# Kernel tuning notes

Hardware: AMD Instinct MI355X
Metric: run time of the kernel (lower is better)

Reference implementation:

```python
import jax, jax.numpy as jnp
from jax import lax
import numpy as np

B, H, W = 16, 512, 512
OPENING_R, EROSION_R, DILATION_R = 5, 2, 1
MIN_SIZE, AREA_THRESHOLD = 2000, 300
INF = np.int32(2 ** 30)


def _disk(r):
    # skimage.morphology.disk: x^2 + y^2 <= r^2 on a (2r+1)^2 grid
    y, x = np.mgrid[-r:r + 1, -r:r + 1]
    return jnp.asarray((x * x + y * y <= r * r).astype(np.float32))


D_OPEN, D_ERODE, D_DILATE = _disk(OPENING_R), _disk(EROSION_R), _disk(DILATION_R)


def _conv2(x, k):
    return lax.conv_general_dilated(x[None, None], k[None, None], (1, 1), 'VALID')[0, 0]


def _erode(fg, se):
    # skimage binary_erosion uses border_value=True (image border does not erode)
    r = se.shape[0] // 2
    x = jnp.pad(fg.astype(jnp.float32), r, constant_values=1.0)
    return _conv2(x, se) >= se.sum() - 0.5


def _dilate(fg, se):
    # skimage binary_dilation uses border_value=False
    r = se.shape[0] // 2
    x = jnp.pad(fg.astype(jnp.float32), r, constant_values=0.0)
    return _conv2(x, se) > 0.5


def _seg_cummin(v, reset, axis, reverse):
    # segmented cumulative-min: scan resets wherever `reset` is True (background)
    def comb(a, b):
        av, af = a
        bv, bf = b
        return jnp.where(bf, bv, jnp.minimum(av, bv)), af | bf

    vv, _ = lax.associative_scan(comb, (v, reset), axis=axis, reverse=reverse)
    return vv


def _label(fg):
    # 4-connectivity connected-component labeling via min-label propagation.
    # Each fg pixel starts with its raveled index; alternating row/col segmented
    # cummin sweeps run under while_loop until a fixed point (root id per comp).
    h, w = fg.shape
    idx = jnp.arange(h * w, dtype=jnp.int32).reshape(h, w)
    lab0 = jnp.where(fg, idx, INF)
    bg = ~fg

    def sweep(l):
        for axis in (1, 0):
            for rev in (False, True):
                l = jnp.where(fg, _seg_cummin(l, bg, axis, rev), INF)
        return l

    def body(c):
        l, _ = c
        nl = sweep(l)
        return nl, jnp.array_equal(nl, l)

    lab, _ = lax.while_loop(lambda c: ~c[1], body, (lab0, jnp.array(False)))
    seg = jnp.where(fg, lab, 0).ravel()
    sizes = jax.ops.segment_sum(fg.astype(jnp.int32).ravel(), seg, num_segments=h * w)
    ncomp = jnp.sum(sizes > 0)
    return lab, sizes, ncomp


def _remove_small_objects(fg, min_size, guard):
    lab, sizes, ncomp = _label(fg)
    px = sizes[jnp.where(fg, lab, 0)]  # component size at every fg pixel
    kept = fg & (px >= min_size)
    # original only removes small objects when label(...).max() > 1
    return jnp.where(ncomp > 1, kept, fg) if guard else kept


def _pipeline(mask):
    fg = mask > 0
    fg = _remove_small_objects(fg, MIN_SIZE, True)
    # remove_small_holes == ~remove_small_objects(~fg, area_threshold + 1)
    fg = ~_remove_small_objects(~fg, AREA_THRESHOLD + 1, False)
    fg = _erode(fg, D_ERODE)
    fg = _dilate(_erode(fg, D_OPEN), D_OPEN)  # binary_opening
    fg = _remove_small_objects(fg, MIN_SIZE, True)
    fg = _dilate(fg, D_DILATE)
    return fg.astype(jnp.float32)  # original casts to int; float32 kept for vjp parity


def setup_inputs() -> dict:
    key = jax.random.key(0)
    # blobby binary masks: threshold bilinearly-upsampled low-res noise so that
    # realistic large connected components (> min_size px) exist
    low = jax.random.uniform(key, (B, H // 16, W // 16), dtype=jnp.float32)
    blob = jax.image.resize(low, (B, H, W), method='bilinear')
    return {'inputs': (blob > 0.5).astype(jnp.float32)}


def reference(inputs):
    return jax.vmap(_pipeline)(inputs)
```

## Files before the change

### kernel.cpp

```cpp
#include <hip/hip_runtime.h>
#include <stdint.h>

#define BATCH 16
#define H 512
#define W 512
#define HW (H * W)
#define NTOT (BATCH * HW)
#define NWORDS (NTOT / 64)

#define TPB 256
#define NBLKW ((NWORDS + TPB - 1) / TPB)

#define SROWS 16
#define SWORDS 128
#define SPIX 8192
#define NSTRIPS (NWORDS / SWORDS)

__device__ __forceinline__ int find_root_c(int* L, int x) {
    int r = x, p = L[r];
    while (p != r) { r = p; p = L[r]; }
    if (L[x] != r) atomicMin(&L[x], r);
    return r;
}

__device__ void merge_uf(int* L, int a, int b) {
    while (true) {
        a = find_root_c(L, a);
        b = find_root_c(L, b);
        if (a == b) return;
        int lo = a < b ? a : b;
        int hi = a < b ? b : a;
        int old = atomicMin(&L[hi], lo);
        if (old == hi) return;
        a = lo; b = old;
    }
}

__device__ __forceinline__ int find_root_lds(int* P, int x) {
    int r = x, p = P[r];
    while (p != r) { r = p; p = P[r]; }
    return r;
}

__device__ void merge_lds(int* P, int a, int b) {
    while (true) {
        a = find_root_lds(P, a);
        b = find_root_lds(P, b);
        if (a == b) return;
        int lo = a < b ? a : b;
        int hi = a < b ? b : a;
        int old = atomicMin(&P[hi], lo);
        if (old == hi) return;
        a = lo; b = old;
    }
}

__device__ __forceinline__ int start_of(uint64_t m, int i, int cv, int base) {
    uint64_t below = i ? ((~m) & ((1ull << i) - 1)) : 0ull;
    if (below == 0) return (cv >= 0) ? cv : base;
    int hz = 63 - __builtin_clzll(below);
    return base + hz + 1;
}

__device__ uint64_t keep_word(const uint64_t* __restrict__ bits,
                              const int* __restrict__ carry, const int* __restrict__ L,
                              const int* __restrict__ sizes, const int* __restrict__ ncomp,
                              int minsz, int gw) {
    uint64_t m = bits[gw];
    uint64_t res = m;
    if (m && ncomp[gw >> 12] > 1) {
        int cv = carry[gw];
        int base = gw << 6;
        while (m) {
            int s = __builtin_ctzll(m);
            uint64_t rest = m >> s;
            uint64_t nr = ~rest;
            int len = nr ? __builtin_ctzll(nr) : (64 - s);
            uint64_t piece = ((len >= 64) ? ~0ull : ((1ull << len) - 1)) << s;
            int start = (s == 0 && cv >= 0) ? cv : (base + s);
            if (sizes[L[start]] < minsz) res &= ~piece;
            m &= ~piece;
        }
    }
    return res;
}

__device__ uint64_t fill_word(const uint64_t* __restrict__ bits,
                              const int* __restrict__ carry, const int* __restrict__ L,
                              const int* __restrict__ sizes, int minsz, int gw) {
    uint64_t fg = bits[gw];
    uint64_t bg = ~fg;
    uint64_t res = fg;
    int cv = carry[gw];
    int base = gw << 6;
    while (bg) {
        int s = __builtin_ctzll(bg);
        uint64_t rest = bg >> s;
        uint64_t nr = ~rest;
        int len = nr ? __builtin_ctzll(nr) : (64 - s);
        uint64_t piece = ((len >= 64) ? ~0ull : ((1ull << len) - 1)) << s;
        int start = (s == 0 && cv >= 0) ? cv : (base + s);
        if (sizes[L[start]] < minsz) res |= piece;
        bg &= ~piece;
    }
    return res;
}

template <int R, bool ERODE>
__device__ uint64_t morph_word_lds(const uint64_t* buf, int lrow, int w, int gyTop) {
    const uint64_t BORDER = ERODE ? ~0ull : 0ull;
    uint64_t res = ERODE ? ~0ull : 0ull;
#pragma unroll
    for (int dy = -R; dy <= R; ++dy) {
        int lr = lrow + dy;
        int gy = gyTop + lr;
        if (gy < 0 || gy >= H) continue;
        int v = R * R - dy * dy;
        int kx = 0;
        while ((kx + 1) * (kx + 1) <= v) ++kx;
        uint64_t cur = buf[lr * 8 + w];
        uint64_t prv = (w > 0) ? buf[lr * 8 + w - 1] : BORDER;
        uint64_t nxt = (w < 7) ? buf[lr * 8 + w + 1] : BORDER;
        uint64_t acc = cur;
#pragma unroll
        for (int dx = 1; dx <= kx; ++dx) {
            uint64_t right = (cur >> dx) | (nxt << (64 - dx));
            uint64_t left  = (cur << dx) | (prv >> (64 - dx));
            if (ERODE) acc &= right & left;
            else       acc |= right | left;
        }
        if (ERODE) res &= acc;
        else       res |= acc;
    }
    return res;
}

__device__ void strip_ccl_body(uint64_t m, uint64_t* sw, int* scarry, int* par,
                               int blk, int t,
                               int* __restrict__ carry, int* __restrict__ L,
                               int* __restrict__ sizes, int* __restrict__ ncomp) {
    sw[t] = m;
    __syncthreads();

    if (t < SROWS) {
        int cv = -1;
        for (int i = 0; i < 8; ++i) {
            int lw = t * 8 + i;
            scarry[lw] = cv;
            uint64_t w = sw[lw];
            if (w >> 63) {
                uint64_t z = ~w;
                if (z == 0) { if (cv < 0) cv = lw << 6; }
                else { int hz = 63 - __builtin_clzll(z); cv = (lw << 6) + hz + 1; }
            } else cv = -1;
        }
    }
    __syncthreads();

    int cv = scarry[t];
    carry[blk * SWORDS + t] = (cv >= 0) ? (blk * SPIX + cv) : -1;
    int lbase = t << 6;
    uint64_t starts = m & ~((m << 1) | ((cv >= 0) ? 1ull : 0ull));
    uint64_t ss = starts;
    while (ss) {
        int s = __builtin_ctzll(ss);
        par[lbase + s] = lbase + s;
        ss &= ss - 1;
    }
    __syncthreads();

    if (t >= 8 && m) {
        uint64_t up = sw[t - 8];
        uint64_t cand = m & up;
        if (cand) {
            uint64_t curprev = (t & 7) ? sw[t - 1] : 0ull;
            uint64_t upprev  = (t & 7) ? sw[t - 9] : 0ull;
            uint64_t curl = (m << 1) | (curprev >> 63);
            uint64_t upl  = (up << 1) | (upprev >> 63);
            cand &= ~(curl & upl);
            int cvu = scarry[t - 8];
            while (cand) {
                int i = __builtin_ctzll(cand);
                int sP = start_of(m, i, cv, lbase);
                int sQ = start_of(up, i, cvu, lbase - 512);
                merge_lds(par, sP, sQ);
                cand &= cand - 1;
            }
        }
    }
    __syncthreads();

    int gpix = blk * SPIX;
    ss = starts;
    while (ss) {
        int s = __builtin_ctzll(ss);
        int ls = lbase + s;
        int r = find_root_lds(par, ls);
        L[gpix + ls] = gpix + r;
        if (r == ls) sizes[gpix + ls] = 0;
        ss &= ss - 1;
    }
    if (t == 0 && (blk & 31) == 0) ncomp[blk >> 5] = 0;
}


__global__ void k_thresh_pack4(const float4* __restrict__ in4,
                               uint64_t* __restrict__ bits) {
    int q = blockIdx.x * blockDim.x + threadIdx.x;
    if (q >= NTOT / 4) return;
    float4 v = in4[q];
    uint32_t nib = (v.x > 0.0f ? 1u : 0u) | (v.y > 0.0f ? 2u : 0u) |
                   (v.z > 0.0f ? 4u : 0u) | (v.w > 0.0f ? 8u : 0u);
    uint64_t val = (uint64_t)nib << (4 * (threadIdx.x & 15));
    val |= __shfl_xor(val, 1);
    val |= __shfl_xor(val, 2);
    val |= __shfl_xor(val, 4);
    val |= __shfl_xor(val, 8);
    if ((threadIdx.x & 15) == 0) bits[q >> 4] = val;
}

__global__ void k_strip_ccl(const uint64_t* __restrict__ bits, int inv,
                            int* __restrict__ carry, int* __restrict__ L,
                            int* __restrict__ sizes, int* __restrict__ ncomp) {
    __shared__ uint64_t sw[SWORDS];
    __shared__ int scarry[SWORDS];
    __shared__ int par[SPIX];
    int blk = blockIdx.x;
    int t = threadIdx.x;
    uint64_t inv64 = inv ? ~0ull : 0ull;
    uint64_t m = bits[blk * SWORDS + t] ^ inv64;
    strip_ccl_body(m, sw, scarry, par, blk, t, carry, L, sizes, ncomp);
}

__global__ void k_keep_strip(const uint64_t* __restrict__ bits,
                             const int* __restrict__ carryIn, const int* __restrict__ Lin,
                             const int* __restrict__ sizesIn, const int* __restrict__ ncompIn,
                             uint64_t* __restrict__ outBits,
                             int* __restrict__ carryOut, int* __restrict__ Lout,
                             int* __restrict__ sizesOut, int* __restrict__ ncompOut) {
    __shared__ uint64_t sw[SWORDS];
    __shared__ int scarry[SWORDS];
    __shared__ int par[SPIX];
    int blk = blockIdx.x;
    int t = threadIdx.x;
    int gw = blk * SWORDS + t;
    uint64_t kw = keep_word(bits, carryIn, Lin, sizesIn, ncompIn, 2000, gw);
    outBits[gw] = kw;
    strip_ccl_body(~kw, sw, scarry, par, blk, t, carryOut, Lout, sizesOut, ncompOut);
}

__global__ void k_merge_bound(const uint64_t* __restrict__ bits, int inv,
                              const int* __restrict__ carry, int* __restrict__ L) {
    int tid = threadIdx.x;
    if (tid >= 248) return;
    int img = blockIdx.x;
    int y = ((tid >> 3) + 1) * SROWS;
    int w = tid & 7;
    int gw = img * 4096 + y * 8 + w;
    uint64_t inv64 = inv ? ~0ull : 0ull;
    uint64_t cur = bits[gw] ^ inv64;
    uint64_t up  = bits[gw - 8] ^ inv64;
    uint64_t cand = cur & up;
    if (!cand) return;
    uint64_t curprev = w ? (bits[gw - 1] ^ inv64) : 0ull;
    uint64_t upprev  = w ? (bits[gw - 9] ^ inv64) : 0ull;
    uint64_t curl = (cur << 1) | (curprev >> 63);
    uint64_t upl  = (up << 1)  | (upprev >> 63);
    cand &= ~(curl & upl);
    if (!cand) return;
    int cvc = carry[gw], cvu = carry[gw - 8];
    int base = gw << 6;
    while (cand) {
        int i = __builtin_ctzll(cand);
        int sP = start_of(cur, i, cvc, base);
        int sQ = start_of(up, i, cvu, base - W);
        merge_uf(L, sP, sQ);
        cand &= cand - 1;
    }
}

__global__ void k_flatten_count(const uint64_t* __restrict__ bits, int inv,
                                const int* __restrict__ carry, int* __restrict__ L,
                                int* __restrict__ sizes, int* __restrict__ ncomp) {
    __shared__ int hk[128];
    __shared__ int hv[128];
    for (int i = threadIdx.x; i < 128; i += TPB) { hk[i] = -1; hv[i] = 0; }
    __syncthreads();

    int gw = blockIdx.x * blockDim.x + threadIdx.x;
    if (gw < NWORDS) {
        uint64_t inv64 = inv ? ~0ull : 0ull;
        uint64_t m = bits[gw] ^ inv64;
        if (m) {
            int cv = carry[gw];
            int base = gw << 6;
            while (m) {
                int s = __builtin_ctzll(m);
                uint64_t rest = m >> s;
                uint64_t nr = ~rest;
                int len = nr ? __builtin_ctzll(nr) : (64 - s);
                uint64_t piece = ((len >= 64) ? ~0ull : ((1ull << len) - 1)) << s;
                bool initial = !(s == 0 && cv >= 0);
                int start = initial ? (base + s) : cv;
                int r = find_root_c(L, start);
                if (initial && r == start) atomicAdd(&ncomp[gw >> 12], 1);
                int cnt = __popcll(piece);
                uint32_t h = ((uint32_t)r * 2654435761u) >> 25;
                bool done = false;
                for (int tt = 0; tt < 16; ++tt) {
                    int slot = (h + tt) & 127;
                    int k = hk[slot];
                    if (k == -1) k = atomicCAS(&hk[slot], -1, r);
                    if (k == -1 || k == r) { atomicAdd(&hv[slot], cnt); done = true; break; }
                }
                if (!done) atomicAdd(&sizes[r], cnt);
                m &= ~piece;
            }
        }
    }
    __syncthreads();
    for (int i = threadIdx.x; i < 128; i += TPB)
        if (hk[i] != -1) atomicAdd(&sizes[hk[i]], hv[i]);
}

__global__ void k_fill_morph_ccl(const uint64_t* __restrict__ bits,
                                 const int* __restrict__ carryB, const int* __restrict__ LB,
                                 const int* __restrict__ sizesB,
                                 uint64_t* __restrict__ bits3,
                                 int* __restrict__ carryA, int* __restrict__ LA,
                                 int* __restrict__ sizesA, int* __restrict__ ncompA) {
    __shared__ uint64_t sw[SWORDS];
    __shared__ int scarry[SWORDS];
    __shared__ union {
        int par[SPIX];
        struct { uint64_t A[320]; uint64_t B[320]; } mo;
    } U;
    int s = blockIdx.x;
    int t = threadIdx.x;
    int img = s >> 5, si = s & 31;
    int gyTop = si * 16 - 12;

    for (int lw = t; lw < 320; lw += SWORDS) {
        int gy = gyTop + (lw >> 3);
        int w = lw & 7;
        uint64_t v = 0;
        if (gy >= 0 && gy < H)
            v = fill_word(bits, carryB, LB, sizesB, 301, img * 4096 + gy * 8 + w);
        U.mo.A[lw] = v;
    }
    __syncthreads();
    for (int lw = t; lw < 320; lw += SWORDS) {
        int lr = lw >> 3;
        if (lr >= 2 && lr <= 37) U.mo.B[lw] = morph_word_lds<2, true>(U.mo.A, lr, lw & 7, gyTop);
    }
    __syncthreads();
    for (int lw = t; lw < 320; lw += SWORDS) {
        int lr = lw >> 3;
        if (lr >= 7 && lr <= 32) U.mo.A[lw] = morph_word_lds<5, true>(U.mo.B, lr, lw & 7, gyTop);
    }
    __syncthreads();
    for (int lw = t; lw < 320; lw += SWORDS) {
        int lr = lw >> 3;
        if (lr >= 12 && lr <= 27) U.mo.B[lw] = morph_word_lds<5, false>(U.mo.A, lr, lw & 7, gyTop);
    }
    __syncthreads();
    uint64_t m3 = U.mo.B[t + 96];
    bits3[s * SWORDS + t] = m3;
    strip_ccl_body(m3, sw, scarry, U.par, s, t, carryA, LA, sizesA, ncompA);
}

__global__ void k_keep_dilate_float(const uint64_t* __restrict__ bits,
                                    const int* __restrict__ carry, const int* __restrict__ L,
                                    const int* __restrict__ sizes, const int* __restrict__ ncomp,
                                    float* __restrict__ out) {
    __shared__ uint64_t kb[10 * 8];
    __shared__ uint64_t db[8 * 8];
    int blk = blockIdx.x;
    int img = blk >> 6;
    int s = blk & 63;
    int y0 = s * 8;
    int t = threadIdx.x;

    if (t < 80) {
        int lr = t >> 3;
        int w = t & 7;
        int gy = y0 - 1 + lr;
        uint64_t v = 0;
        if (gy >= 0 && gy < H)
            v = keep_word(bits, carry, L, sizes, ncomp, 2000, img * 4096 + gy * 8 + w);
        kb[t] = v;
    }
    __syncthreads();
    if (t < 64) {
        int r = t >> 3, w = t & 7;
        uint64_t cur = kb[(r + 1) * 8 + w];
        uint64_t up  = kb[r * 8 + w];
        uint64_t dn  = kb[(r + 2) * 8 + w];
        uint64_t prv = w ? kb[(r + 1) * 8 + w - 1] : 0ull;
        uint64_t nxt = (w < 7) ? kb[(r + 1) * 8 + w + 1] : 0ull;
        db[t] = cur | up | dn | (cur << 1) | (prv >> 63) | (cur >> 1) | (nxt << 63);
    }
    __syncthreads();

    int q0 = t * 16;
    uint64_t wd = db[q0 >> 6];
    int sh = q0 & 63;
    float4* o = (float4*)(out + (size_t)img * HW + (size_t)y0 * W + q0);
#pragma unroll
    for (int k = 0; k < 4; ++k) {
        uint32_t nib = (uint32_t)(wd >> (sh + k * 4)) & 0xFu;
        float4 f;
        f.x = (nib & 1u) ? 1.0f : 0.0f;
        f.y = (nib & 2u) ? 1.0f : 0.0f;
        f.z = (nib & 4u) ? 1.0f : 0.0f;
        f.w = (nib & 8u) ? 1.0f : 0.0f;
        o[k] = f;
    }
}

extern "C" void kernel_launch(void* const* d_in, const int* in_sizes, int n_in,
                              void* d_out, int out_size, void* d_ws, size_t ws_size,
                              hipStream_t stream) {
    const float* in = (const float*)d_in[0];
    float* out = (float*)d_out;

    uint8_t* ws = (uint8_t*)d_ws;
    int* LA      = (int*)ws;
    int* sizesA  = (int*)(ws + (size_t)NTOT * 4);
    int* LB      = (int*)(ws + (size_t)NTOT * 8);
    int* sizesB  = (int*)(ws + (size_t)NTOT * 12);
    uint64_t* bits1 = (uint64_t*)(ws + (size_t)NTOT * 16);
    uint64_t* bits2 = bits1 + NWORDS;
    uint64_t* bits3 = bits2 + NWORDS;
    int* carryA = (int*)(bits3 + NWORDS);
    int* carryB = carryA + NWORDS;
    int* ncompA = carryB + NWORDS;
    int* ncompB = ncompA + BATCH;

    k_thresh_pack4<<<(NTOT / 4 + TPB - 1) / TPB, TPB, 0, stream>>>((const float4*)in, bits1);

    k_strip_ccl<<<NSTRIPS, SWORDS, 0, stream>>>(bits1, 0, carryA, LA, sizesA, ncompA);
    k_merge_bound<<<BATCH, 256, 0, stream>>>(bits1, 0, carryA, LA);
    k_flatten_count<<<NBLKW, TPB, 0, stream>>>(bits1, 0, carryA, LA, sizesA, ncompA);

    k_keep_strip<<<NSTRIPS, SWORDS, 0, stream>>>(bits1, carryA, LA, sizesA, ncompA,
                                                 bits2, carryB, LB, sizesB, ncompB);
    k_merge_bound<<<BATCH, 256, 0, stream>>>(bits2, 1, carryB, LB);
    k_flatten_count<<<NBLKW, TPB, 0, stream>>>(bits2, 1, carryB, LB, sizesB, ncompB);

    k_fill_morph_ccl<<<NSTRIPS, SWORDS, 0, stream>>>(bits2, carryB, LB, sizesB,
                                                     bits3, carryA, LA, sizesA, ncompA);
    k_merge_bound<<<BATCH, 256, 0, stream>>>(bits3, 0, carryA, LA);
    k_flatten_count<<<NBLKW, TPB, 0, stream>>>(bits3, 0, carryA, LA, sizesA, ncompA);

    k_keep_dilate_float<<<BATCH * 64, TPB, 0, stream>>>(bits3, carryA, LA, sizesA, ncompA, out);
}
```

Baseline: 201.3 us.

## Fuse all pipeline stages into one cooperative kernel with grid syncs

Replaces eleven separate kernel launches with a single cooperative persistent kernel of 512 blocks. Stages are separated by grid.sync(), and shared memory is reused through a union. The aim is to remove per-launch overhead and inter-kernel gaps, since the workload is small. In exchange, each stage runs under a fixed 512-block geometry, boundary merges are spread as 8 items per block, and every grid barrier has its own cost. The old multi-kernel path stays as a fallback if the cooperative launch fails.

```diff
diff --git a/kernel.cpp b/kernel.cpp
--- a/kernel.cpp
+++ b/kernel.cpp
@@ -1,5 +1,8 @@
 #include <hip/hip_runtime.h>
+#include <hip/hip_cooperative_groups.h>
 #include <stdint.h>
+
+namespace cg = cooperative_groups;
 
 #define BATCH 16
 #define H 512
@@ -15,6 +18,7 @@
 #define SWORDS 128
 #define SPIX 8192
 #define NSTRIPS (NWORDS / SWORDS)
+#define NBOUND (BATCH * 248)
 
 __device__ __forceinline__ int find_root_c(int* L, int x) {
     int r = x, p = L[r];
@@ -139,7 +143,7 @@
                                int blk, int t,
                                int* __restrict__ carry, int* __restrict__ L,
                                int* __restrict__ sizes, int* __restrict__ ncomp) {
-    sw[t] = m;
+    if (t < SWORDS) sw[t] = m;
     __syncthreads();
 
     if (t < SROWS) {
@@ -157,19 +161,23 @@
     }
     __syncthreads();
 
-    int cv = scarry[t];
-    carry[blk * SWORDS + t] = (cv >= 0) ? (blk * SPIX + cv) : -1;
     int lbase = t << 6;
-    uint64_t starts = m & ~((m << 1) | ((cv >= 0) ? 1ull : 0ull));
-    uint64_t ss = starts;
-    while (ss) {
-        int s = __builtin_ctzll(ss);
-        par[lbase + s] = lbase + s;
-        ss &= ss - 1;
-    }
-    __syncthreads();
-
-    if (t >= 8 && m) {
+    int cv = -1;
+    uint64_t starts = 0ull;
+    if (t < SWORDS) {
+        cv = scarry[t];
+        carry[blk * SWORDS + t] = (cv >= 0) ? (blk * SPIX + cv) : -1;
+        starts = m & ~((m << 1) | ((cv >= 0) ? 1ull : 0ull));
+        uint64_t ss = starts;
+        while (ss) {
+            int s = __builtin_ctzll(ss);
+            par[lbase + s] = lbase + s;
+            ss &= ss - 1;
+        }
+    }
+    __syncthreads();
+
+    if (t >= 8 && t < SWORDS && m) {
         uint64_t up = sw[t - 8];
         uint64_t cand = m & up;
         if (cand) {
@@ -190,74 +198,24 @@
     }
     __syncthreads();
 
-    int gpix = blk * SPIX;
-    ss = starts;
-    while (ss) {
-        int s = __builtin_ctzll(ss);
-        int ls = lbase + s;
-        int r = find_root_lds(par, ls);
-        L[gpix + ls] = gpix + r;
-        if (r == ls) sizes[gpix + ls] = 0;
-        ss &= ss - 1;
+    if (t < SWORDS) {
+        int gpix = blk * SPIX;
+        uint64_t ss = starts;
+        while (ss) {
+            int s = __builtin_ctzll(ss);
+            int ls = lbase + s;
+            int r = find_root_lds(par, ls);
+            L[gpix + ls] = gpix + r;
+            if (r == ls) sizes[gpix + ls] = 0;
+            ss &= ss - 1;
+        }
     }
     if (t == 0 && (blk & 31) == 0) ncomp[blk >> 5] = 0;
 }
 
-
-__global__ void k_thresh_pack4(const float4* __restrict__ in4,
-                               uint64_t* __restrict__ bits) {
-    int q = blockIdx.x * blockDim.x + threadIdx.x;
-    if (q >= NTOT / 4) return;
-    float4 v = in4[q];
-    uint32_t nib = (v.x > 0.0f ? 1u : 0u) | (v.y > 0.0f ? 2u : 0u) |
-                   (v.z > 0.0f ? 4u : 0u) | (v.w > 0.0f ? 8u : 0u);
-    uint64_t val = (uint64_t)nib << (4 * (threadIdx.x & 15));
-    val |= __shfl_xor(val, 1);
-    val |= __shfl_xor(val, 2);
-    val |= __shfl_xor(val, 4);
-    val |= __shfl_xor(val, 8);
-    if ((threadIdx.x & 15) == 0) bits[q >> 4] = val;
-}
-
-__global__ void k_strip_ccl(const uint64_t* __restrict__ bits, int inv,
-                            int* __restrict__ carry, int* __restrict__ L,
-                            int* __restrict__ sizes, int* __restrict__ ncomp) {
-    __shared__ uint64_t sw[SWORDS];
-    __shared__ int scarry[SWORDS];
-    __shared__ int par[SPIX];
-    int blk = blockIdx.x;
-    int t = threadIdx.x;
-    uint64_t inv64 = inv ? ~0ull : 0ull;
-    uint64_t m = bits[blk * SWORDS + t] ^ inv64;
-    strip_ccl_body(m, sw, scarry, par, blk, t, carry, L, sizes, ncomp);
-}
-
-__global__ void k_keep_strip(const uint64_t* __restrict__ bits,
-                             const int* __restrict__ carryIn, const int* __restrict__ Lin,
-                             const int* __restrict__ sizesIn, const int* __restrict__ ncompIn,
-                             uint64_t* __restrict__ outBits,
-                             int* __restrict__ carryOut, int* __restrict__ Lout,
-                             int* __restrict__ sizesOut, int* __restrict__ ncompOut) {
-    __shared__ uint64_t sw[SWORDS];
-    __shared__ int scarry[SWORDS];
-    __shared__ int par[SPIX];
-    int blk = blockIdx.x;
-    int t = threadIdx.x;
-    int gw = blk * SWORDS + t;
-    uint64_t kw = keep_word(bits, carryIn, Lin, sizesIn, ncompIn, 2000, gw);
-    outBits[gw] = kw;
-    strip_ccl_body(~kw, sw, scarry, par, blk, t, carryOut, Lout, sizesOut, ncompOut);
-}
-
-__global__ void k_merge_bound(const uint64_t* __restrict__ bits, int inv,
-                              const int* __restrict__ carry, int* __restrict__ L) {
-    int tid = threadIdx.x;
-    if (tid >= 248) return;
-    int img = blockIdx.x;
-    int y = ((tid >> 3) + 1) * SROWS;
-    int w = tid & 7;
-    int gw = img * 4096 + y * 8 + w;
-    uint64_t inv64 = inv ? ~0ull : 0ull;
+__device__ void merge_bound_item(const uint64_t* __restrict__ bits, uint64_t inv64,
+                                 const int* __restrict__ carry, int* __restrict__ L,
+                                 int gw, int w) {
     uint64_t cur = bits[gw] ^ inv64;
     uint64_t up  = bits[gw - 8] ^ inv64;
     uint64_t cand = cur & up;
@@ -277,6 +235,283 @@
         merge_uf(L, sP, sQ);
         cand &= cand - 1;
     }
+}
+
+__device__ void flatten_block(const uint64_t* __restrict__ bits, uint64_t inv64,
+                              const int* __restrict__ carry, int* __restrict__ L,
+                              int* __restrict__ sizes, int* __restrict__ ncomp,
+                              int blk, int t, int* hk, int* hv) {
+    if (t < 128) { hk[t] = -1; hv[t] = 0; }
+    __syncthreads();
+    if (t < SWORDS) {
+        int gw = blk * SWORDS + t;
+        uint64_t m = bits[gw] ^ inv64;
+        if (m) {
+            int cv = carry[gw];
+            int base = gw << 6;
+            while (m) {
+                int s = __builtin_ctzll(m);
+                uint64_t rest = m >> s;
+                uint64_t nr = ~rest;
+                int len = nr ? __builtin_ctzll(nr) : (64 - s);
+                uint64_t piece = ((len >= 64) ? ~0ull : ((1ull << len) - 1)) << s;
+                bool initial = !(s == 0 && cv >= 0);
+                int start = initial ? (base + s) : cv;
+                int r = find_root_c(L, start);
+                if (initial && r == start) atomicAdd(&ncomp[gw >> 12], 1);
+                int cnt = __popcll(piece);
+                uint32_t h = ((uint32_t)r * 2654435761u) >> 25;
+                bool done = false;
+                for (int tt = 0; tt < 16; ++tt) {
+                    int slot = (h + tt) & 127;
+                    int k = hk[slot];
+                    if (k == -1) k = atomicCAS(&hk[slot], -1, r);
+                    if (k == -1 || k == r) { atomicAdd(&hv[slot], cnt); done = true; break; }
+                }
+                if (!done) atomicAdd(&sizes[r], cnt);
+                m &= ~piece;
+            }
+        }
+    }
+    __syncthreads();
+    if (t < 128 && hk[t] != -1) atomicAdd(&sizes[hk[t]], hv[t]);
+}
+
+__device__ void keep_dilate_seg(const uint64_t* __restrict__ bits,
+                                const int* __restrict__ carry, const int* __restrict__ L,
+                                const int* __restrict__ sizes, const int* __restrict__ ncomp,
+                                float* __restrict__ out,
+                                int img, int y0, int t, uint64_t* kb, uint64_t* db) {
+    if (t < 80) {
+        int lr = t >> 3;
+        int w = t & 7;
+        int gy = y0 - 1 + lr;
+        uint64_t v = 0;
+        if (gy >= 0 && gy < H)
+            v = keep_word(bits, carry, L, sizes, ncomp, 2000, img * 4096 + gy * 8 + w);
+        kb[t] = v;
+    }
+    __syncthreads();
+    if (t < 64) {
+        int r = t >> 3, w = t & 7;
+        uint64_t cur = kb[(r + 1) * 8 + w];
+        uint64_t up  = kb[r * 8 + w];
+        uint64_t dn  = kb[(r + 2) * 8 + w];
+        uint64_t prv = w ? kb[(r + 1) * 8 + w - 1] : 0ull;
+        uint64_t nxt = (w < 7) ? kb[(r + 1) * 8 + w + 1] : 0ull;
+        db[t] = cur | up | dn | (cur << 1) | (prv >> 63) | (cur >> 1) | (nxt << 63);
+    }
+    __syncthreads();
+
+    int q0 = t * 16;
+    uint64_t wd = db[q0 >> 6];
+    int sh = q0 & 63;
+    float4* o = (float4*)(out + (size_t)img * HW + (size_t)y0 * W + q0);
+#pragma unroll
+    for (int k = 0; k < 4; ++k) {
+        uint32_t nib = (uint32_t)(wd >> (sh + k * 4)) & 0xFu;
+        float4 f;
+        f.x = (nib & 1u) ? 1.0f : 0.0f;
+        f.y = (nib & 2u) ? 1.0f : 0.0f;
+        f.z = (nib & 4u) ? 1.0f : 0.0f;
+        f.w = (nib & 8u) ? 1.0f : 0.0f;
+        o[k] = f;
+    }
+}
+
+__global__ __launch_bounds__(256, 2) void k_mega(
+        const float4* __restrict__ in4, float* __restrict__ out,
+        int* LA, int* sizesA, int* LB, int* sizesB,
+        uint64_t* bits1, uint64_t* bits2, uint64_t* bits3,
+        int* carryA, int* carryB, int* ncompA, int* ncompB) {
+    cg::grid_group grid = cg::this_grid();
+    __shared__ uint64_t sw[SWORDS];
+    __shared__ int scarry[SWORDS];
+    __shared__ union US {
+        int par[SPIX];
+        struct { uint64_t A[320]; uint64_t B[320]; } mo;
+        struct { int hk[128]; int hv[128]; } ha;
+        struct { uint64_t kb[80]; uint64_t db[64]; } kd;
+    } U;
+    int blk = blockIdx.x;
+    int t = threadIdx.x;
+    int tid = blk * 256 + t;
+
+#pragma unroll
+    for (int it = 0; it < 8; ++it) {
+        int q = it * (NSTRIPS * 256) + tid;
+        float4 v = in4[q];
+        uint32_t nib = (v.x > 0.0f ? 1u : 0u) | (v.y > 0.0f ? 2u : 0u) |
+                       (v.z > 0.0f ? 4u : 0u) | (v.w > 0.0f ? 8u : 0u);
+        uint64_t val = (uint64_t)nib << (4 * (t & 15));
+        val |= __shfl_xor(val, 1);
+        val |= __shfl_xor(val, 2);
+        val |= __shfl_xor(val, 4);
+        val |= __shfl_xor(val, 8);
+        if ((t & 15) == 0) bits1[q >> 4] = val;
+    }
+    grid.sync();
+
+    {
+        uint64_t m = (t < SWORDS) ? bits1[blk * SWORDS + t] : 0ull;
+        strip_ccl_body(m, sw, scarry, U.par, blk, t, carryA, LA, sizesA, ncompA);
+    }
+    grid.sync();
+
+    if (t < 8) {
+        int item = blk * 8 + t;
+        if (item < NBOUND) {
+            int img = item / 248;
+            int r = item - img * 248;
+            int gw = img * 4096 + ((r >> 3) + 1) * SROWS * 8 + (r & 7);
+            merge_bound_item(bits1, 0ull, carryA, LA, gw, r & 7);
+        }
+    }
+    grid.sync();
+
+    flatten_block(bits1, 0ull, carryA, LA, sizesA, ncompA, blk, t, U.ha.hk, U.ha.hv);
+    grid.sync();
+
+    {
+        uint64_t m = 0ull;
+        if (t < SWORDS) {
+            int gw = blk * SWORDS + t;
+            uint64_t kw = keep_word(bits1, carryA, LA, sizesA, ncompA, 2000, gw);
+            bits2[gw] = kw;
+            m = ~kw;
+        }
+        strip_ccl_body(m, sw, scarry, U.par, blk, t, carryB, LB, sizesB, ncompB);
+    }
+    grid.sync();
+
+    if (t < 8) {
+        int item = blk * 8 + t;
+        if (item < NBOUND) {
+            int img = item / 248;
+            int r = item - img * 248;
+            int gw = img * 4096 + ((r >> 3) + 1) * SROWS * 8 + (r & 7);
+            merge_bound_item(bits2, ~0ull, carryB, LB, gw, r & 7);
+        }
+    }
+    grid.sync();
+
+    flatten_block(bits2, ~0ull, carryB, LB, sizesB, ncompB, blk, t, U.ha.hk, U.ha.hv);
+    grid.sync();
+
+    {
+        int img = blk >> 5, si = blk & 31;
+        int gyTop = si * 16 - 12;
+        for (int lw = t; lw < 320; lw += 256) {
+            int gy = gyTop + (lw >> 3);
+            int w = lw & 7;
+            uint64_t v = 0;
+            if (gy >= 0 && gy < H)
+                v = fill_word(bits2, carryB, LB, sizesB, 301, img * 4096 + gy * 8 + w);
+            U.mo.A[lw] = v;
+        }
+        __syncthreads();
+        for (int lw = t; lw < 320; lw += 256) {
+            int lr = lw >> 3;
+            if (lr >= 2 && lr <= 37) U.mo.B[lw] = morph_word_lds<2, true>(U.mo.A, lr, lw & 7, gyTop);
+        }
+        __syncthreads();
+        for (int lw = t; lw < 320; lw += 256) {
+            int lr = lw >> 3;
+            if (lr >= 7 && lr <= 32) U.mo.A[lw] = morph_word_lds<5, true>(U.mo.B, lr, lw & 7, gyTop);
+        }
+        __syncthreads();
+        for (int lw = t; lw < 320; lw += 256) {
+            int lr = lw >> 3;
+            if (lr >= 12 && lr <= 27) U.mo.B[lw] = morph_word_lds<5, false>(U.mo.A, lr, lw & 7, gyTop);
+        }
+        __syncthreads();
+        uint64_t m3 = 0ull;
+        if (t < SWORDS) {
+            m3 = U.mo.B[t + 96];
+            bits3[blk * SWORDS + t] = m3;
+        }
+        strip_ccl_body(m3, sw, scarry, U.par, blk, t, carryA, LA, sizesA, ncompA);
+    }
+    grid.sync();
+
+    if (t < 8) {
+        int item = blk * 8 + t;
+        if (item < NBOUND) {
+            int img = item / 248;
+            int r = item - img * 248;
+            int gw = img * 4096 + ((r >> 3) + 1) * SROWS * 8 + (r & 7);
+            merge_bound_item(bits3, 0ull, carryA, LA, gw, r & 7);
+        }
+    }
+    grid.sync();
+
+    flatten_block(bits3, 0ull, carryA, LA, sizesA, ncompA, blk, t, U.ha.hk, U.ha.hv);
+    grid.sync();
+
+    for (int k = 0; k < 2; ++k) {
+        int seg = blk * 2 + k;
+        int img = seg >> 6, s8 = seg & 63;
+        keep_dilate_seg(bits3, carryA, LA, sizesA, ncompA, out,
+                        img, s8 * 8, t, U.kd.kb, U.kd.db);
+        __syncthreads();
+    }
+}
+
+__global__ void k_thresh_pack4(const float4* __restrict__ in4,
+                               uint64_t* __restrict__ bits) {
+    int q = blockIdx.x * blockDim.x + threadIdx.x;
+    if (q >= NTOT / 4) return;
+    float4 v = in4[q];
+    uint32_t nib = (v.x > 0.0f ? 1u : 0u) | (v.y > 0.0f ? 2u : 0u) |
+                   (v.z > 0.0f ? 4u : 0u) | (v.w > 0.0f ? 8u : 0u);
+    uint64_t val = (uint64_t)nib << (4 * (threadIdx.x & 15));
+    val |= __shfl_xor(val, 1);
+    val |= __shfl_xor(val, 2);
+    val |= __shfl_xor(val, 4);
+    val |= __shfl_xor(val, 8);
+    if ((threadIdx.x & 15) == 0) bits[q >> 4] = val;
+}
+
+__global__ void k_strip_ccl(const uint64_t* __restrict__ bits, int inv,
+                            int* __restrict__ carry, int* __restrict__ L,
+                            int* __restrict__ sizes, int* __restrict__ ncomp) {
+    __shared__ uint64_t sw[SWORDS];
+    __shared__ int scarry[SWORDS];
+    __shared__ int par[SPIX];
+    int blk = blockIdx.x;
+    int t = threadIdx.x;
+    uint64_t inv64 = inv ? ~0ull : 0ull;
+    uint64_t m = bits[blk * SWORDS + t] ^ inv64;
+    strip_ccl_body(m, sw, scarry, par, blk, t, carry, L, sizes, ncomp);
+}
+
+__global__ void k_keep_strip(const uint64_t* __restrict__ bits,
+                             const int* __restrict__ carryIn, const int* __restrict__ Lin,
+                             const int* __restrict__ sizesIn, const int* __restrict__ ncompIn,
+                             uint64_t* __restrict__ outBits,
+                             int* __restrict__ carryOut, int* __restrict__ Lout,
+                             int* __restrict__ sizesOut, int* __restrict__ ncompOut) {
+    __shared__ uint64_t sw[SWORDS];
+    __shared__ int scarry[SWORDS];
+    __shared__ int par[SPIX];
+    int blk = blockIdx.x;
+    int t = threadIdx.x;
+    int gw = blk * SWORDS + t;
+    uint64_t kw = keep_word(bits, carryIn, Lin, sizesIn, ncompIn, 2000, gw);
+    outBits[gw] = kw;
+    strip_ccl_body(~kw, sw, scarry, par, blk, t, carryOut, Lout, sizesOut, ncompOut);
+}
+
+__global__ void k_merge_bound(const uint64_t* __restrict__ bits, int inv,
+                              const int* __restrict__ carry, int* __restrict__ L) {
+    int tid = threadIdx.x;
+    if (tid >= 248) return;
+    int img = blockIdx.x;
+    int y = ((tid >> 3) + 1) * SROWS;
+    int w = tid & 7;
+    int gw = img * 4096 + y * 8 + w;
+    uint64_t inv64 = inv ? ~0ull : 0ull;
+    merge_bound_item(bits, inv64, carry, L, gw, w);
 }
 
 __global__ void k_flatten_count(const uint64_t* __restrict__ bits, int inv,
@@ -378,44 +613,7 @@
     int blk = blockIdx.x;
     int img = blk >> 6;
     int s = blk & 63;
-    int y0 = s * 8;
-    int t = threadIdx.x;
-
-    if (t < 80) {
-        int lr = t >> 3;
-        int w = t & 7;
-        int gy = y0 - 1 + lr;
-        uint64_t v = 0;
-        if (gy >= 0 && gy < H)
-            v = keep_word(bits, carry, L, sizes, ncomp, 2000, img * 4096 + gy * 8 + w);
-        kb[t] = v;
-    }
-    __syncthreads();
-    if (t < 64) {
-        int r = t >> 3, w = t & 7;
-        uint64_t cur = kb[(r + 1) * 8 + w];
-        uint64_t up  = kb[r * 8 + w];
-        uint64_t dn  = kb[(r + 2) * 8 + w];
-        uint64_t prv = w ? kb[(r + 1) * 8 + w - 1] : 0ull;
-        uint64_t nxt = (w < 7) ? kb[(r + 1) * 8 + w + 1] : 0ull;
-        db[t] = cur | up | dn | (cur << 1) | (prv >> 63) | (cur >> 1) | (nxt << 63);
-    }
-    __syncthreads();
-
-    int q0 = t * 16;
-    uint64_t wd = db[q0 >> 6];
-    int sh = q0 & 63;
-    float4* o = (float4*)(out + (size_t)img * HW + (size_t)y0 * W + q0);
-#pragma unroll
-    for (int k = 0; k < 4; ++k) {
-        uint32_t nib = (uint32_t)(wd >> (sh + k * 4)) & 0xFu;
-        float4 f;
-        f.x = (nib & 1u) ? 1.0f : 0.0f;
-        f.y = (nib & 2u) ? 1.0f : 0.0f;
-        f.z = (nib & 4u) ? 1.0f : 0.0f;
-        f.w = (nib & 8u) ? 1.0f : 0.0f;
-        o[k] = f;
-    }
+    keep_dilate_seg(bits, carry, L, sizes, ncomp, out, img, s * 8, threadIdx.x, kb, db);
 }
 
 extern "C" void kernel_launch(void* const* d_in, const int* in_sizes, int n_in,
@@ -437,21 +635,27 @@
     int* ncompA = carryB + NWORDS;
     int* ncompB = ncompA + BATCH;
 
-    k_thresh_pack4<<<(NTOT / 4 + TPB - 1) / TPB, TPB, 0, stream>>>((const float4*)in, bits1);
-
-    k_strip_ccl<<<NSTRIPS, SWORDS, 0, stream>>>(bits1, 0, carryA, LA, sizesA, ncompA);
-    k_merge_bound<<<BATCH, 256, 0, stream>>>(bits1, 0, carryA, LA);
-    k_flatten_count<<<NBLKW, TPB, 0, stream>>>(bits1, 0, carryA, LA, sizesA, ncompA);
-
-    k_keep_strip<<<NSTRIPS, SWORDS, 0, stream>>>(bits1, carryA, LA, sizesA, ncompA,
-                                                 bits2, carryB, LB, sizesB, ncompB);
-    k_merge_bound<<<BATCH, 256, 0, stream>>>(bits2, 1, carryB, LB);
-    k_flatten_count<<<NBLKW, TPB, 0, stream>>>(bits2, 1, carryB, LB, sizesB, ncompB);
-
-    k_fill_morph_ccl<<<NSTRIPS, SWORDS, 0, stream>>>(bits2, carryB, LB, sizesB,
-                                                     bits3, carryA, LA, sizesA, ncompA);
-    k_merge_bound<<<BATCH, 256, 0, stream>>>(bits3, 0, carryA, LA);
-    k_flatten_count<<<NBLKW, TPB, 0, stream>>>(bits3, 0, carryA, LA, sizesA, ncompA);
-
-    k_keep_dilate_float<<<BATCH * 64, TPB, 0, stream>>>(bits3, carryA, LA, sizesA, ncompA, out);
-}
+    const float4* in4 = (const float4*)in;
+    void* args[] = { (void*)&in4, (void*)&out, (void*)&LA, (void*)&sizesA,
+                     (void*)&LB, (void*)&sizesB, (void*)&bits1, (void*)&bits2,
+                     (void*)&bits3, (void*)&carryA, (void*)&carryB,
+                     (void*)&ncompA, (void*)&ncompB };
+    hipError_t err = hipLaunchCooperativeKernel((const void*)k_mega, dim3(NSTRIPS),
+                                                dim3(256), (void**)args, 0, stream);
+    if (err != hipSuccess) {
+        (void)hipGetLastError();
+        k_thresh_pack4<<<(NTOT / 4 + TPB - 1) / TPB, TPB, 0, stream>>>((const float4*)in, bits1);
+        k_strip_ccl<<<NSTRIPS, SWORDS, 0, stream>>>(bits1, 0, carryA, LA, sizesA, ncompA);
+        k_merge_bound<<<BATCH, 256, 0, stream>>>(bits1, 0, carryA, LA);
+        k_flatten_count<<<NBLKW, TPB, 0, stream>>>(bits1, 0, carryA, LA, sizesA, ncompA);
+        k_keep_strip<<<NSTRIPS, SWORDS, 0, stream>>>(bits1, carryA, LA, sizesA, ncompA,
+                                                     bits2, carryB, LB, sizesB, ncompB);
+        k_merge_bound<<<BATCH, 256, 0, stream>>>(bits2, 1, carryB, LB);
+        k_flatten_count<<<NBLKW, TPB, 0, stream>>>(bits2, 1, carryB, LB, sizesB, ncompB);
+        k_fill_morph_ccl<<<NSTRIPS, SWORDS, 0, stream>>>(bits2, carryB, LB, sizesB,
+                                                         bits3, carryA, LA, sizesA, ncompA);
+        k_merge_bound<<<BATCH, 256, 0, stream>>>(bits3, 0, carryA, LA);
+        k_flatten_count<<<NBLKW, TPB, 0, stream>>>(bits3, 0, carryA, LA, sizesA, ncompA);
+        k_keep_dilate_float<<<BATCH * 64, TPB, 0, stream>>>(bits3, carryA, LA, sizesA, ncompA, out);
+    }
+}
```

After: 721.0 us. +258.2%, slower.
